# Performance work log

Hardware: AMD Instinct MI355X
Metric: run time of the kernel (lower is better)

The kernel has to match this reference:

```python
import jax, jax.numpy as jnp
import numpy as np

LAM_CONSIST = 0.1
LAM_LR = 1.0
LAM_PAIR = 1.0


def _cubic(x, a=-0.75):
    # PyTorch bicubic kernel (a = -0.75)
    ax = jnp.abs(x)
    ax2 = ax * ax
    ax3 = ax2 * ax
    f1 = (a + 2.0) * ax3 - (a + 3.0) * ax2 + 1.0
    f2 = a * ax3 - 5.0 * a * ax2 + 8.0 * a * ax - 4.0 * a
    return jnp.where(ax <= 1.0, f1, jnp.where(ax < 2.0, f2, 0.0))


def _resize_matrix(in_size: int, out_size: int) -> jnp.ndarray:
    """Weight matrix [out_size, in_size] for antialiased bicubic resize
    (align_corners=False, antialias=True, border replicate) as in
    F.interpolate(..., mode='bicubic', antialias=True)."""
    scale = in_size / out_size
    s_aa = max(scale, 1.0)  # widen kernel when downscaling (antialias)
    support = 2.0 * s_aa
    ext = int(np.ceil(support)) + 1
    centers = (np.arange(out_size, dtype=np.float64) + 0.5) * scale - 0.5
    idx = np.arange(-ext, in_size + ext)
    dist = (idx[None, :] - centers[:, None]) / s_aa  # [out, in+2ext]
    w = _cubic(jnp.asarray(dist, dtype=jnp.float32))
    w = w / jnp.sum(w, axis=1, keepdims=True)  # torch normalizes window weights
    idx_c = np.clip(idx, 0, in_size - 1)  # clamp -> replicate border
    M = jnp.zeros((out_size, in_size), dtype=jnp.float32).at[:, idx_c].add(w)
    return M


def _resize_bicubic_aa(img: jnp.ndarray, th: int, tw: int) -> jnp.ndarray:
    # img: [B, C, H, W] -> [B, C, th, tw], separable resize via two matmuls
    _, _, h, w = img.shape
    Mh = _resize_matrix(h, th)  # [th, h]
    Mw = _resize_matrix(w, tw)  # [tw, w]
    return jnp.einsum('oh,bchw,pw->bcop', Mh, img, Mw)


def setup_inputs() -> dict:
    key = jax.random.key(0)
    k1, k2, k3 = jax.random.split(key, 3)
    pred_hr = jax.random.normal(k1, (32, 3, 512, 512), dtype=jnp.float32)
    target_hr = jax.random.normal(k2, (32, 3, 512, 512), dtype=jnp.float32)
    lr_ref = jax.random.normal(k3, (32, 3, 128, 128), dtype=jnp.float32)
    scale = jnp.full((32,), 4.0, dtype=jnp.float32)  # uniform -> static sizes
    return {"pred_hr": pred_hr, "target_hr": target_hr, "lr_ref": lr_ref, "scale": scale}


def reference(pred_hr, target_hr, lr_ref, scale):
    pix = jnp.mean(jnp.abs(pred_hr - target_hr))
    # project_scale(pred_hr, src=scale, dst=1): uniform scale=4 ->
    # target size == lr_ref spatial size (static, read from lr_ref shape)
    th, tw = lr_ref.shape[-2], lr_ref.shape[-1]
    pred_lr = _resize_bicubic_aa(pred_hr, th, tw)
    lr_term = jnp.mean(jnp.abs(pred_lr - lr_ref))
    pair_term = jnp.float32(0.0)  # pair_pred_hr / pair_scale are None
    consist = LAM_LR * lr_term + LAM_PAIR * pair_term
    total = pix + LAM_CONSIST * consist
    return (total, pix, consist, lr_term, pair_term)
```

## Files before the change

kernel.cpp:

```cpp
#include <hip/hip_runtime.h>

#define HW    512
#define OUTW  128
#define NIMG  96
#define N_HR  ((long long)NIMG*HW*HW)
#define N_LR  ((long long)NIMG*OUTW*OUTW)
#define NPART (NIMG*32)

__device__ __forceinline__ float cubic075(float x){
    float ax = fabsf(x);
    float ax2 = ax*ax, ax3 = ax2*ax;
    const float A = -0.75f;
    float f1 = (A+2.f)*ax3 - (A+3.f)*ax2 + 1.f;
    float f2 = A*ax3 - 5.f*A*ax2 + 8.f*A*ax - 4.f*A;
    return ax <= 1.f ? f1 : (ax < 2.f ? f2 : 0.f);
}

__device__ __forceinline__ void get_weights(float w[16]){
    float s = 0.f;
#pragma unroll
    for (int k = 0; k < 16; ++k){
        float d = ((float)k - 7.5f) * 0.25f;
        w[k] = cubic075(d);
        s += w[k];
    }
#pragma unroll
    for (int k = 0; k < 16; ++k) w[k] /= s;
}

__global__ __launch_bounds__(256) void kmain(const float* __restrict__ pred,
                                             const float* __restrict__ tgt,
                                             const float* __restrict__ lr,
                                             double* __restrict__ part){
    const int img = blockIdx.x >> 3;
    const int tid = threadIdx.x;
    const int w   = tid >> 6;
    const int l   = tid & 63;
    const int gw  = ((blockIdx.x & 7) << 2) + w;
    const int o0  = gw << 2;
    const int s   = (gw << 4) - 6;

    float wt[16]; get_weights(wt);
    const float* P = pred + (size_t)img * (HW*HW);
    const float* T = tgt  + (size_t)img * (HW*HW);
    const float* L = lr   + (size_t)img * (OUTW*OUTW);

    float acc[4][2] = {{0.f,0.f},{0.f,0.f},{0.f,0.f},{0.f,0.f}};
    float pix_acc = 0.f, lr_acc = 0.f;

    int r0 = min(HW-1, max(0, s + 0));
    int r1 = min(HW-1, max(0, s + 1));
    const float4* rp0 = (const float4*)(P + (size_t)r0 * HW);
    const float4* rp1 = (const float4*)(P + (size_t)r1 * HW);
    float4 c0 = rp0[2*l], c1 = rp0[2*l+1];
    float4 n0 = rp1[2*l], n1 = rp1[2*l+1];
    float4 tc0, tc1, tn0, tn1;

#pragma unroll 4
    for (int i = 0; i < 28; ++i){
        float4 f0, f1, tf0, tf1;
        if (i < 26){
            int rn = min(HW-1, max(0, s + i + 2));
            const float4* rp = (const float4*)(P + (size_t)rn * HW);
            f0 = rp[2*l]; f1 = rp[2*l+1];
        }
        if (i + 2 >= 6 && i + 2 < 22){
            const float4* tp = (const float4*)(T + (size_t)(s + i + 2) * HW);
            tf0 = tp[2*l]; tf1 = tp[2*l+1];
        }

        const float p0=c0.x,p1v=c0.y,p2v=c0.z,p3=c0.w,
                    p4=c1.x,p5=c1.y,p6=c1.z,p7=c1.w;

        if (i >= 6 && i < 22){
            pix_acc += fabsf(p0-tc0.x)+fabsf(p1v-tc0.y)+fabsf(p2v-tc0.z)+fabsf(p3-tc0.w)
                     + fabsf(p4-tc1.x)+fabsf(p5-tc1.y)+fabsf(p6-tc1.z)+fabsf(p7-tc1.w);
        }

        float Lm6 = __shfl_up(p2v,1,64), Lm5 = __shfl_up(p3,1,64),
              Lm4 = __shfl_up(p4,1,64),  Lm3 = __shfl_up(p5,1,64),
              Lm2 = __shfl_up(p6,1,64),  Lm1 = __shfl_up(p7,1,64);
        float R8  = __shfl_down(p0,1,64), R9  = __shfl_down(p1v,1,64),
              R10 = __shfl_down(p2v,1,64),R11 = __shfl_down(p3,1,64),
              R12 = __shfl_down(p4,1,64), R13 = __shfl_down(p5,1,64);
        if (l == 0){ Lm6=p0; Lm5=p0; Lm4=p0; Lm3=p0; Lm2=p0; Lm1=p0; }
        if (l == 63){ R8=p7; R9=p7; R10=p7; R11=p7; R12=p7; R13=p7; }

        float w20[20] = {Lm6,Lm5,Lm4,Lm3,Lm2,Lm1,p0,p1v,p2v,p3,p4,p5,p6,p7,
                         R8,R9,R10,R11,R12,R13};
        float h0 = 0.f, h1 = 0.f;
#pragma unroll
        for (int k = 0; k < 16; ++k){
            h0 += wt[k]*w20[k];
            h1 += wt[k]*w20[k+4];
        }

#pragma unroll
        for (int q = 0; q < 4; ++q){
            int k = i - 4*q;
            if (k >= 0 && k < 16){
                acc[q][0] += wt[k]*h0;
                acc[q][1] += wt[k]*h1;
            }
        }

        c0=n0; c1=n1; n0=f0; n1=f1;
        tc0=tn0; tc1=tn1; tn0=tf0; tn1=tf1;
    }

#pragma unroll
    for (int q = 0; q < 4; ++q){
        const float2 lv = *(const float2*)(L + (size_t)(o0+q)*OUTW + 2*l);
        lr_acc += fabsf(acc[q][0]-lv.x) + fabsf(acc[q][1]-lv.y);
    }

#pragma unroll
    for (int off = 32; off > 0; off >>= 1){
        pix_acc += __shfl_down(pix_acc, off, 64);
        lr_acc  += __shfl_down(lr_acc,  off, 64);
    }
    if (l == 0){
        const int slot = (blockIdx.x << 2) + w;
        part[slot]         = (double)pix_acc;
        part[NPART + slot] = (double)lr_acc;
    }
}

__global__ __launch_bounds__(256) void k3(const double* __restrict__ part,
                                          float* __restrict__ out){
    const int t = threadIdx.x;
    double v1 = 0.0, v2 = 0.0;
    for (int i = t; i < NPART; i += 256){
        v1 += part[i];
        v2 += part[NPART + i];
    }
#pragma unroll
    for (int off = 32; off > 0; off >>= 1){
        v1 += __shfl_down(v1, off, 64);
        v2 += __shfl_down(v2, off, 64);
    }
    __shared__ double s1[4], s2[4];
    const int lane = t & 63, wid = t >> 6;
    if (lane == 0){ s1[wid] = v1; s2[wid] = v2; }
    __syncthreads();
    if (t == 0){
        double S1 = s1[0]+s1[1]+s1[2]+s1[3];
        double S2 = s2[0]+s2[1]+s2[2]+s2[3];
        float pix     = (float)(S1 / (double)N_HR);
        float lr_term = (float)(S2 / (double)N_LR);
        float pair    = 0.f;
        float consist = 1.0f * lr_term + 1.0f * pair;
        float total   = pix + 0.1f * consist;
        out[0] = total; out[1] = pix; out[2] = consist; out[3] = lr_term; out[4] = pair;
    }
}

extern "C" void kernel_launch(void* const* d_in, const int* in_sizes, int n_in,
                              void* d_out, int out_size, void* d_ws, size_t ws_size,
                              hipStream_t stream){
    const float* pred = (const float*)d_in[0];
    const float* tgt  = (const float*)d_in[1];
    const float* lrr  = (const float*)d_in[2];
    float* out = (float*)d_out;

    double* part = (double*)d_ws;

    kmain<<<NIMG*8, 256, 0, stream>>>(pred, tgt, lrr, part);
    k3<<<1, 256, 0, stream>>>(part, out);
}
```

Measured before the change: 229.5 us.

## Share horizontal-pass rows across waves via LDS ring buffer in resize kernel

```diff
diff --git a/kernel.cpp b/kernel.cpp
--- a/kernel.cpp
+++ b/kernel.cpp
@@ -5,7 +5,7 @@
 #define NIMG  96
 #define N_HR  ((long long)NIMG*HW*HW)
 #define N_LR  ((long long)NIMG*OUTW*OUTW)
-#define NPART (NIMG*32)
+#define NBLK  (NIMG*8)
 
 __device__ __forceinline__ float cubic075(float x){
     float ax = fabsf(x);
@@ -28,51 +28,61 @@
     for (int k = 0; k < 16; ++k) w[k] /= s;
 }
 
-__global__ __launch_bounds__(256) void kmain(const float* __restrict__ pred,
-                                             const float* __restrict__ tgt,
-                                             const float* __restrict__ lr,
-                                             double* __restrict__ part){
-    const int img = blockIdx.x >> 3;
+__global__ __launch_bounds__(256, 3) void kmain(const float* __restrict__ pred,
+                                                const float* __restrict__ tgt,
+                                                const float* __restrict__ lr,
+                                                double* __restrict__ part1,
+                                                double* __restrict__ part2){
+    const int b   = blockIdx.x;
+    const int W   = ((b & 7) * (NBLK/8)) + (b >> 3);
+    const int img = W >> 3;
+    const int grp = W & 7;
+    const int o0  = grp << 4;
+    const int s   = (o0 << 2) - 6;
     const int tid = threadIdx.x;
     const int w   = tid >> 6;
     const int l   = tid & 63;
-    const int gw  = ((blockIdx.x & 7) << 2) + w;
-    const int o0  = gw << 2;
-    const int s   = (gw << 4) - 6;
+
+    __shared__ float  ring[32][128];
+    __shared__ double sred[8];
 
     float wt[16]; get_weights(wt);
     const float* P = pred + (size_t)img * (HW*HW);
     const float* T = tgt  + (size_t)img * (HW*HW);
     const float* L = lr   + (size_t)img * (OUTW*OUTW);
 
-    float acc[4][2] = {{0.f,0.f},{0.f,0.f},{0.f,0.f},{0.f,0.f}};
     float pix_acc = 0.f, lr_acc = 0.f;
 
-    int r0 = min(HW-1, max(0, s + 0));
-    int r1 = min(HW-1, max(0, s + 1));
+    int r0 = min(HW-1, max(0, s + w));
+    int r1 = min(HW-1, max(0, s + 4 + w));
     const float4* rp0 = (const float4*)(P + (size_t)r0 * HW);
     const float4* rp1 = (const float4*)(P + (size_t)r1 * HW);
     float4 c0 = rp0[2*l], c1 = rp0[2*l+1];
     float4 n0 = rp1[2*l], n1 = rp1[2*l+1];
     float4 tc0, tc1, tn0, tn1;
+    if (w >= 2){
+        const float4* tp = (const float4*)(T + (size_t)(s + 4 + w) * HW);
+        tn0 = tp[2*l]; tn1 = tp[2*l+1];
+    }
 
-#pragma unroll 4
-    for (int i = 0; i < 28; ++i){
+    for (int i = 0; i < 19; ++i){
+        const int jcur = 4*i + w;
+        const int j2   = jcur + 8;
         float4 f0, f1, tf0, tf1;
-        if (i < 26){
-            int rn = min(HW-1, max(0, s + i + 2));
+        if (i < 17){
+            int rn = min(HW-1, max(0, s + j2));
             const float4* rp = (const float4*)(P + (size_t)rn * HW);
             f0 = rp[2*l]; f1 = rp[2*l+1];
         }
-        if (i + 2 >= 6 && i + 2 < 22){
-            const float4* tp = (const float4*)(T + (size_t)(s + i + 2) * HW);
+        if (j2 < 70){
+            const float4* tp = (const float4*)(T + (size_t)(s + j2) * HW);
             tf0 = tp[2*l]; tf1 = tp[2*l+1];
         }
 
         const float p0=c0.x,p1v=c0.y,p2v=c0.z,p3=c0.w,
                     p4=c1.x,p5=c1.y,p6=c1.z,p7=c1.w;
 
-        if (i >= 6 && i < 22){
+        if (jcur >= 6 && jcur < 70){
             pix_acc += fabsf(p0-tc0.x)+fabsf(p1v-tc0.y)+fabsf(p2v-tc0.z)+fabsf(p3-tc0.w)
                      + fabsf(p4-tc1.x)+fabsf(p5-tc1.y)+fabsf(p6-tc1.z)+fabsf(p7-tc1.w);
         }
@@ -94,14 +104,18 @@
             h0 += wt[k]*w20[k];
             h1 += wt[k]*w20[k+4];
         }
+        float2 st; st.x = h0; st.y = h1;
+        *(float2*)&ring[jcur & 31][2*l] = st;
 
+        __syncthreads();
+
+        if (i >= 3 && tid < 128){
+            const int q = i - 3;
+            float acc = 0.f;
 #pragma unroll
-        for (int q = 0; q < 4; ++q){
-            int k = i - 4*q;
-            if (k >= 0 && k < 16){
-                acc[q][0] += wt[k]*h0;
-                acc[q][1] += wt[k]*h1;
-            }
+            for (int r = 0; r < 16; ++r)
+                acc += wt[r] * ring[(4*q + r) & 31][tid];
+            lr_acc += fabsf(acc - L[(size_t)(o0 + q) * OUTW + tid]);
         }
 
         c0=n0; c1=n1; n0=f0; n1=f1;
@@ -109,30 +123,24 @@
     }
 
 #pragma unroll
-    for (int q = 0; q < 4; ++q){
-        const float2 lv = *(const float2*)(L + (size_t)(o0+q)*OUTW + 2*l);
-        lr_acc += fabsf(acc[q][0]-lv.x) + fabsf(acc[q][1]-lv.y);
-    }
-
-#pragma unroll
     for (int off = 32; off > 0; off >>= 1){
         pix_acc += __shfl_down(pix_acc, off, 64);
         lr_acc  += __shfl_down(lr_acc,  off, 64);
     }
-    if (l == 0){
-        const int slot = (blockIdx.x << 2) + w;
-        part[slot]         = (double)pix_acc;
-        part[NPART + slot] = (double)lr_acc;
-    }
+    if (l == 0){ sred[w] = (double)pix_acc; sred[4+w] = (double)lr_acc; }
+    __syncthreads();
+    if (tid == 0)  part1[b] = sred[0]+sred[1]+sred[2]+sred[3];
+    if (tid == 64) part2[b] = sred[4]+sred[5]+sred[6]+sred[7];
 }
 
-__global__ __launch_bounds__(256) void k3(const double* __restrict__ part,
+__global__ __launch_bounds__(256) void k3(const double* __restrict__ part1,
+                                          const double* __restrict__ part2,
                                           float* __restrict__ out){
     const int t = threadIdx.x;
     double v1 = 0.0, v2 = 0.0;
-    for (int i = t; i < NPART; i += 256){
-        v1 += part[i];
-        v2 += part[NPART + i];
+    for (int i = t; i < NBLK; i += 256){
+        v1 += part1[i];
+        v2 += part2[i];
     }
 #pragma unroll
     for (int off = 32; off > 0; off >>= 1){
@@ -163,8 +171,9 @@
     const float* lrr  = (const float*)d_in[2];
     float* out = (float*)d_out;
 
-    double* part = (double*)d_ws;
+    double* part1 = (double*)d_ws;
+    double* part2 = part1 + NBLK;
 
-    kmain<<<NIMG*8, 256, 0, stream>>>(pred, tgt, lrr, part);
-    k3<<<1, 256, 0, stream>>>(part, out);
+    kmain<<<NBLK, 256, 0, stream>>>(pred, tgt, lrr, part1, part2);
+    k3<<<1, 256, 0, stream>>>(part1, part2, out);
 }
```

After: 233.0 us. Within noise of the previous version (+1.5%).
